# Kernel optimization log

Hardware: AMD Instinct MI355X
Metric: run time of the kernel (lower is better)

The kernel has to match this reference:

```python
import jax, jax.numpy as jnp
import numpy as np

B, V, C, H, W, D = 1, 3, 64, 96, 96, 48


def bilinear_sample(feat, gx, gy):
    """torch F.grid_sample(mode='bilinear', padding_mode='zeros', align_corners=True).
    feat: (B, C, H, W); gx, gy: (B, N) normalized coords in [-1, 1]. Returns (B, C, N)."""
    Bf, Cf, Hf, Wf = feat.shape
    x = (gx + 1.0) * 0.5 * (Wf - 1)
    y = (gy + 1.0) * 0.5 * (Hf - 1)
    x0 = jnp.floor(x)
    y0 = jnp.floor(y)
    wx1 = x - x0
    wy1 = y - y0
    wx0 = 1.0 - wx1
    wy0 = 1.0 - wy1
    flat = feat.reshape(Bf, Cf, Hf * Wf)

    def gather(xi, yi):
        valid = (xi >= 0) & (xi <= Wf - 1) & (yi >= 0) & (yi <= Hf - 1)
        xi_c = jnp.clip(xi, 0, Wf - 1).astype(jnp.int32)
        yi_c = jnp.clip(yi, 0, Hf - 1).astype(jnp.int32)
        idx = (yi_c * Wf + xi_c)[:, None, :]  # (B,1,N), broadcast over C
        return jnp.take_along_axis(flat, idx, axis=2) * valid[:, None, :]

    out = (gather(x0, y0) * (wx0 * wy0)[:, None]
           + gather(x0 + 1, y0) * (wx1 * wy0)[:, None]
           + gather(x0, y0 + 1) * (wx0 * wy1)[:, None]
           + gather(x0 + 1, y0 + 1) * (wx1 * wy1)[:, None])
    return out


def src_grid(proj_mat, depth_values, Hs, Ws):
    """homo_warp grid computation. proj_mat: (B,3,4); depth_values: (B,D).
    Returns normalized gx, gy each of shape (B, D*Hs*Ws)."""
    xs = jnp.arange(Ws, dtype=jnp.float32)
    ys = jnp.arange(Hs, dtype=jnp.float32)
    gx_, gy_ = jnp.meshgrid(xs, ys)  # (Hs, Ws) each
    ref = jnp.stack([gx_.ravel(), gy_.ravel(), jnp.ones(Hs * Ws, jnp.float32)], 0)  # (3, HW)
    R = proj_mat[:, :, :3]
    T = proj_mat[:, :, 3]
    # (B,3,D,HW): R @ p + T / depth
    pts = jnp.einsum('bij,jn->bin', R, ref)[:, :, None, :] + T[:, :, None, None] / depth_values[:, None, :, None]
    xy = pts[:, :2] / pts[:, 2:3]
    gx = xy[:, 0] / ((Ws - 1) / 2.0) - 1.0
    gy = xy[:, 1] / ((Hs - 1) / 2.0) - 1.0
    Bb = proj_mat.shape[0]
    return gx.reshape(Bb, -1), gy.reshape(Bb, -1)


def setup_inputs() -> dict:
    key = jax.random.key(0)
    k1, k2, k3, k4 = jax.random.split(key, 4)
    imgs = jax.random.normal(k1, (B, V, 3, H, W), jnp.float32)
    feats = jax.random.normal(k2, (B, V, C, H, W), jnp.float32)
    # near-identity projections so warped coords land mostly in-range (z ~ 1)
    eye = jnp.broadcast_to(jnp.eye(3, dtype=jnp.float32), (B, V, 3, 3))
    Rn = eye + 0.05 * jax.random.normal(k3, (B, V, 3, 3), jnp.float32)
    Tn = 0.5 * jax.random.normal(jax.random.fold_in(k3, 1), (B, V, 3, 1), jnp.float32)
    proj_mats = jnp.concatenate([Rn, Tn], axis=-1)
    depth_values = 2.0 + 4.0 * jax.random.uniform(k4, (B, D), jnp.float32)
    return {"imgs": imgs, "feats": feats, "proj_mats": proj_mats, "depth_values": depth_values}


def reference(imgs, feats, proj_mats, depth_values):
    Bb, Vv, _, Hh, Ww = imgs.shape
    Cc = feats.shape[2]
    Dd = depth_values.shape[1]
    # ref view volume (broadcast over D)
    ref_volume = jnp.broadcast_to(feats[:, 0][:, :, None], (Bb, Cc, Dd, Hh, Ww))
    volume_sum = ref_volume
    volume_sq_sum = ref_volume ** 2
    mask_sum = jnp.ones((Bb, Dd, Hh, Ww), jnp.float32)  # ref view always in-range
    img_chans = [jnp.broadcast_to(imgs[:, 0][:, :, None], (Bb, 3, Dd, Hh, Ww))]
    for i in range(Vv - 1):  # small fixed number of source views
        gx, gy = src_grid(proj_mats[:, i + 1], depth_values, Hh, Ww)
        wv = bilinear_sample(feats[:, i + 1], gx, gy).reshape(Bb, Cc, Dd, Hh, Ww)
        wi = bilinear_sample(imgs[:, i + 1], gx, gy).reshape(Bb, 3, Dd, Hh, Ww)
        m = ((gx > -1.0) & (gx < 1.0) & (gy > -1.0) & (gy < 1.0)).astype(jnp.float32).reshape(Bb, Dd, Hh, Ww)
        volume_sum = volume_sum + wv
        volume_sq_sum = volume_sq_sum + wv ** 2
        mask_sum = mask_sum + m
        img_chans.append(wi)
    count = 1.0 / mask_sum[:, None]  # (B,1,D,H,W)
    var = volume_sq_sum * count - (volume_sum * count) ** 2  # (B,C,D,H,W)
    img_chans.append(var)
    return jnp.concatenate(img_chans, axis=1)  # (B, 3*V + C, D, H, W)
```

## Files before the change

### kernel.cpp

```cpp
#include <hip/hip_runtime.h>

#define BDIM 256

constexpr int Vv = 3, Cc = 64, Hh = 96, Ww = 96, Dd = 48;
constexpr int HW = Hh * Ww;
constexpr int NPIX = Dd * HW;
constexpr int DHW = Dd * HW;

__device__ __forceinline__ void compute_warp_v(const float* __restrict__ P, float depth,
                                               float xf, float yf,
                                               int offs[4], float wts[4], float& inbf)
{
#pragma clang fp contract(off)
    const float r00 = P[0], r01 = P[1], r02 = P[2],  t0 = P[3];
    const float r10 = P[4], r11 = P[5], r12 = P[6],  t1 = P[7];
    const float r20 = P[8], r21 = P[9], r22 = P[10], t2 = P[11];

    const float px = ((r00 * xf + r01 * yf) + r02) + t0 / depth;
    const float py = ((r10 * xf + r11 * yf) + r12) + t1 / depth;
    const float pz = ((r20 * xf + r21 * yf) + r22) + t2 / depth;

    const float xy0 = px / pz;
    const float xy1 = py / pz;
    const float gx = xy0 / ((float)(Ww - 1) * 0.5f) - 1.0f;
    const float gy = xy1 / ((float)(Hh - 1) * 0.5f) - 1.0f;

    const bool inb = (gx > -1.0f) && (gx < 1.0f) && (gy > -1.0f) && (gy < 1.0f);
    inbf = inb ? 1.0f : 0.0f;

    const float sx = (gx + 1.0f) * 0.5f * (float)(Ww - 1);
    const float sy = (gy + 1.0f) * 0.5f * (float)(Hh - 1);
    const float x0 = floorf(sx), y0 = floorf(sy);
    const float wx1 = sx - x0, wy1 = sy - y0;
    const float wx0 = 1.0f - wx1, wy0 = 1.0f - wy1;

#pragma unroll
    for (int k = 0; k < 4; ++k) {
        const float xi = (k & 1) ? (x0 + 1.0f) : x0;
        const float yi = (k & 2) ? (y0 + 1.0f) : y0;
        const float wk = ((k & 1) ? wx1 : wx0) * ((k & 2) ? wy1 : wy0);
        const bool valid = (xi >= 0.0f) && (xi <= (float)(Ww - 1)) &&
                           (yi >= 0.0f) && (yi <= (float)(Hh - 1));
        const float xc = fminf(fmaxf(xi, 0.0f), (float)(Ww - 1));
        const float yc = fminf(fmaxf(yi, 0.0f), (float)(Hh - 1));
        offs[k] = (int)yc * Ww + (int)xc;
        wts[k] = valid ? wk : 0.0f;
    }
}

__device__ __forceinline__ void compute_warp(const float* __restrict__ proj, float depth,
                                             float xf, float yf,
                                             int offs[2][4], float wts[2][4], float& msum)
{
    msum = 1.0f;
#pragma unroll
    for (int v = 0; v < 2; ++v) {
        float inb;
        compute_warp_v(proj + (v + 1) * 12, depth, xf, yf, offs[v], wts[v], inb);
        msum += inb;
    }
}

__device__ __forceinline__ float var_one(float fr, float a1, float a2, float cnt)
{
    const float s  = fr + a1 + a2;
    const float q  = fr * fr + a1 * a1 + a2 * a2;
    const float sc = s * cnt;
    return q * cnt - sc * sc;
}

__global__ void __launch_bounds__(BDIM) transpose_feats_kernel(const float* __restrict__ feats,
                                                               float* __restrict__ ft)
{
    __shared__ float tile[64][65];
    const int v  = blockIdx.y;
    const int p0 = blockIdx.x * 64;
    const float* src = feats + (size_t)v * Cc * HW;

    const int px = threadIdx.x & 63;
    const int c0 = threadIdx.x >> 6;
#pragma unroll
    for (int c = c0; c < Cc; c += 4)
        tile[c][px] = src[(size_t)c * HW + p0 + px];
    __syncthreads();

    const int cc  = threadIdx.x & 63;
    const int pr0 = threadIdx.x >> 6;
    float* dst = ft + ((size_t)v * HW + p0) * Cc;
#pragma unroll
    for (int p = pr0; p < 64; p += 4)
        dst[p * Cc + cc] = tile[cc][p];
}

__global__ void __launch_bounds__(BDIM) ge_row_kernel(
    const float* __restrict__ imgs, const float* __restrict__ ftr,
    const float* __restrict__ proj, const float* __restrict__ depthv,
    float* __restrict__ out)
{
    __shared__ float s_tile[2][Cc / 2][Ww + 1];
    __shared__ alignas(16) int   s_base[2][2][Ww][4];
    __shared__ alignas(16) float s_wt[2][2][Ww][4];
    __shared__ float s_inb[2][2][Ww];

    const int blk = blockIdx.x;
    const int h   = blk / (Dd / 2);
    const int dq  = blk - h * (Dd / 2);
    const int d0  = dq * 2;
    const int tid = threadIdx.x;
    const int rowb0 = d0 * HW + h * Ww;

    if (tid < 2 * Ww) {
        const int v = (tid >= Ww) ? 1 : 0;
        const int w = tid - v * Ww;
        const float* ib = imgs + (size_t)(v + 1) * 3 * HW;
#pragma unroll
        for (int dd = 0; dd < 2; ++dd) {
            int offs[4];
            float wts[4];
            float inb;
            compute_warp_v(proj + (v + 1) * 12, depthv[d0 + dd], (float)w, (float)h,
                           offs, wts, inb);
            s_inb[v][dd][w] = inb;
#pragma unroll
            for (int k = 0; k < 4; ++k) {
                s_base[v][dd][w][k] = ((v + 1) * HW + offs[k]) * Cc;
                s_wt[v][dd][w][k]   = wts[k];
            }
#pragma unroll
            for (int c = 0; c < 3; ++c) {
                const float* p = ib + (size_t)c * HW;
                const float acc = wts[0] * p[offs[0]] + wts[1] * p[offs[1]] +
                                  wts[2] * p[offs[2]] + wts[3] * p[offs[3]];
                out[(3 * (v + 1) + c) * DHW + rowb0 + dd * HW + w] = acc;
            }
        }
    }
    if (tid < Ww) {
        const int hw = h * Ww + tid;
#pragma unroll
        for (int c = 0; c < 3; ++c) {
            const float val = imgs[c * HW + hw];
            out[c * DHW + rowb0 + tid]      = val;
            out[c * DHW + rowb0 + HW + tid] = val;
        }
    }
    __syncthreads();

    const int wave = tid >> 6;
    const int lane = tid & 63;
    const int sub  = lane >> 3;
    const int cq   = lane & 7;
    const int c4   = cq << 2;
    const int p0   = wave * (Ww / 4);

#pragma unroll
    for (int hc = 0; hc < 2; ++hc) {
        const int ch0 = hc * (Cc / 2);

        for (int i = 0; i < 3; ++i) {
            const int p = p0 + i * 8 + sub;
            const int4   b00 = *reinterpret_cast<const int4*>(&s_base[0][0][p][0]);
            const int4   b10 = *reinterpret_cast<const int4*>(&s_base[1][0][p][0]);
            const int4   b01 = *reinterpret_cast<const int4*>(&s_base[0][1][p][0]);
            const int4   b11 = *reinterpret_cast<const int4*>(&s_base[1][1][p][0]);
            const float4 w00 = *reinterpret_cast<const float4*>(&s_wt[0][0][p][0]);
            const float4 w10 = *reinterpret_cast<const float4*>(&s_wt[1][0][p][0]);
            const float4 w01 = *reinterpret_cast<const float4*>(&s_wt[0][1][p][0]);
            const float4 w11 = *reinterpret_cast<const float4*>(&s_wt[1][1][p][0]);
            const float cnt0 = 1.0f / (1.0f + s_inb[0][0][p] + s_inb[1][0][p]);
            const float cnt1 = 1.0f / (1.0f + s_inb[0][1][p] + s_inb[1][1][p]);

            const float4 fr = *reinterpret_cast<const float4*>(
                ftr + (size_t)(h * Ww + p) * Cc + ch0 + c4);

            const float4 a00 = *reinterpret_cast<const float4*>(ftr + b00.x + ch0 + c4);
            const float4 a01 = *reinterpret_cast<const float4*>(ftr + b00.y + ch0 + c4);
            const float4 a02 = *reinterpret_cast<const float4*>(ftr + b00.z + ch0 + c4);
            const float4 a03 = *reinterpret_cast<const float4*>(ftr + b00.w + ch0 + c4);
            const float4 a10 = *reinterpret_cast<const float4*>(ftr + b10.x + ch0 + c4);
            const float4 a11 = *reinterpret_cast<const float4*>(ftr + b10.y + ch0 + c4);
            const float4 a12 = *reinterpret_cast<const float4*>(ftr + b10.z + ch0 + c4);
            const float4 a13 = *reinterpret_cast<const float4*>(ftr + b10.w + ch0 + c4);
            const float4 c00 = *reinterpret_cast<const float4*>(ftr + b01.x + ch0 + c4);
            const float4 c01 = *reinterpret_cast<const float4*>(ftr + b01.y + ch0 + c4);
            const float4 c02 = *reinterpret_cast<const float4*>(ftr + b01.z + ch0 + c4);
            const float4 c03 = *reinterpret_cast<const float4*>(ftr + b01.w + ch0 + c4);
            const float4 c10 = *reinterpret_cast<const float4*>(ftr + b11.x + ch0 + c4);
            const float4 c11 = *reinterpret_cast<const float4*>(ftr + b11.y + ch0 + c4);
            const float4 c12 = *reinterpret_cast<const float4*>(ftr + b11.z + ch0 + c4);
            const float4 c13 = *reinterpret_cast<const float4*>(ftr + b11.w + ch0 + c4);

#define VAR_LANE(dd, W0, W1, V0a, V0b, V0c, V0d, V1a, V1b, V1c, V1d, CNT)                 \
            {                                                                              \
                {                                                                          \
                    const float a1 = W0.x * V0a.x + W0.y * V0b.x + W0.z * V0c.x + W0.w * V0d.x; \
                    const float a2 = W1.x * V1a.x + W1.y * V1b.x + W1.z * V1c.x + W1.w * V1d.x; \
                    s_tile[dd][c4 + 0][p] = var_one(fr.x, a1, a2, CNT);                    \
                }                                                                          \
                {                                                                          \
                    const float a1 = W0.x * V0a.y + W0.y * V0b.y + W0.z * V0c.y + W0.w * V0d.y; \
                    const float a2 = W1.x * V1a.y + W1.y * V1b.y + W1.z * V1c.y + W1.w * V1d.y; \
                    s_tile[dd][c4 + 1][p] = var_one(fr.y, a1, a2, CNT);                    \
                }                                                                          \
                {                                                                          \
                    const float a1 = W0.x * V0a.z + W0.y * V0b.z + W0.z * V0c.z + W0.w * V0d.z; \
                    const float a2 = W1.x * V1a.z + W1.y * V1b.z + W1.z * V1c.z + W1.w * V1d.z; \
                    s_tile[dd][c4 + 2][p] = var_one(fr.z, a1, a2, CNT);                    \
                }                                                                          \
                {                                                                          \
                    const float a1 = W0.x * V0a.w + W0.y * V0b.w + W0.z * V0c.w + W0.w * V0d.w; \
                    const float a2 = W1.x * V1a.w + W1.y * V1b.w + W1.z * V1c.w + W1.w * V1d.w; \
                    s_tile[dd][c4 + 3][p] = var_one(fr.w, a1, a2, CNT);                    \
                }                                                                          \
            }

            VAR_LANE(0, w00, w10, a00, a01, a02, a03, a10, a11, a12, a13, cnt0)
            VAR_LANE(1, w01, w11, c00, c01, c02, c03, c10, c11, c12, c13, cnt1)
#undef VAR_LANE
        }
        __syncthreads();

#pragma unroll
        for (int j = 0; j < (2 * (Cc / 2) * Ww) / BDIM; ++j) {
            const int idx = tid + j * BDIM;
            const int dd  = idx / ((Cc / 2) * Ww);
            const int r   = idx - dd * ((Cc / 2) * Ww);
            const int cc  = r / Ww;
            const int p   = r - cc * Ww;
            out[(9 + ch0 + cc) * DHW + rowb0 + dd * HW + p] = s_tile[dd][cc][p];
        }
        __syncthreads();
    }
}

__global__ void __launch_bounds__(BDIM) ge_direct_kernel(
    const float* __restrict__ imgs, const float* __restrict__ feats,
    const float* __restrict__ proj, const float* __restrict__ depthv,
    float* __restrict__ out)
{
    const int idx = blockIdx.x * BDIM + threadIdx.x;
    if (idx >= NPIX) return;
    const int w = idx % Ww;
    const int t = idx / Ww;
    const int h = t % Hh;
    const int d = t / Hh;
    const int ohw = h * Ww + w;

    int offs[2][4];
    float wts[2][4];
    float msum;
    compute_warp(proj, depthv[d], (float)w, (float)h, offs, wts, msum);

    const int obase = d * HW + ohw;
#pragma unroll
    for (int c = 0; c < 3; ++c)
        out[c * DHW + obase] = imgs[c * HW + ohw];

#pragma unroll
    for (int v = 0; v < 2; ++v) {
        const float* ib = imgs + (size_t)(v + 1) * 3 * HW;
#pragma unroll
        for (int c = 0; c < 3; ++c) {
            const float* p = ib + (size_t)c * HW;
            const float acc = wts[v][0] * p[offs[v][0]] + wts[v][1] * p[offs[v][1]] +
                              wts[v][2] * p[offs[v][2]] + wts[v][3] * p[offs[v][3]];
            out[(3 * (v + 1) + c) * DHW + obase] = acc;
        }
    }

    const float count = 1.0f / msum;
    const float* f0 = feats;
    const float* f1 = feats + (size_t)Cc * HW;
    const float* f2 = feats + (size_t)2 * Cc * HW;
#pragma unroll 8
    for (int c = 0; c < Cc; ++c) {
        const float fr = f0[(size_t)c * HW + ohw];
        const float* p1 = f1 + (size_t)c * HW;
        const float* p2 = f2 + (size_t)c * HW;
        const float a1 = wts[0][0] * p1[offs[0][0]] + wts[0][1] * p1[offs[0][1]] +
                         wts[0][2] * p1[offs[0][2]] + wts[0][3] * p1[offs[0][3]];
        const float a2 = wts[1][0] * p2[offs[1][0]] + wts[1][1] * p2[offs[1][1]] +
                         wts[1][2] * p2[offs[1][2]] + wts[1][3] * p2[offs[1][3]];
        const float s = fr + a1 + a2;
        const float sq = fr * fr + a1 * a1 + a2 * a2;
        const float sc = s * count;
        out[(3 * Vv + c) * DHW + obase] = sq * count - sc * sc;
    }
}

extern "C" void kernel_launch(void* const* d_in, const int* in_sizes, int n_in,
                              void* d_out, int out_size, void* d_ws, size_t ws_size,
                              hipStream_t stream)
{
    const float* imgs   = (const float*)d_in[0];
    const float* feats  = (const float*)d_in[1];
    const float* proj   = (const float*)d_in[2];
    const float* depthv = (const float*)d_in[3];
    float* out = (float*)d_out;

    const size_t need = (size_t)Vv * HW * Cc * sizeof(float);

    if (ws_size >= need) {
        float* ftr = (float*)d_ws;
        dim3 g1(HW / 64, Vv);
        transpose_feats_kernel<<<g1, BDIM, 0, stream>>>(feats, ftr);
        ge_row_kernel<<<Hh * (Dd / 2), BDIM, 0, stream>>>(imgs, ftr, proj, depthv, out);
    } else {
        const int blocks = (NPIX + BDIM - 1) / BDIM;
        ge_direct_kernel<<<blocks, BDIM, 0, stream>>>(imgs, feats, proj, depthv, out);
    }
}
```

Baseline: 174.6 us.

## Halve shared tile and split depth loop to raise row-kernel occupancy

The variance tile in shared memory is halved by processing the two depth slices one after another instead of together. Each inner iteration now issues 9 gathered float4 loads instead of 17. A launch-bounds hint asks for 5 blocks per CU. The warp-setup phase is spread over all 256 threads instead of 192, with each thread handling one (view, depth, column) item. The aim is lower register and LDS pressure for higher occupancy, at the cost of twice as many barriers and less memory-level parallelism per thread.

```diff
diff --git a/kernel.cpp b/kernel.cpp
--- a/kernel.cpp
+++ b/kernel.cpp
@@ -92,12 +92,12 @@
         dst[p * Cc + cc] = tile[cc][p];
 }
 
-__global__ void __launch_bounds__(BDIM) ge_row_kernel(
+__global__ void __launch_bounds__(BDIM, 5) ge_row_kernel(
     const float* __restrict__ imgs, const float* __restrict__ ftr,
     const float* __restrict__ proj, const float* __restrict__ depthv,
     float* __restrict__ out)
 {
-    __shared__ float s_tile[2][Cc / 2][Ww + 1];
+    __shared__ float s_tile[Cc / 2][Ww + 1];
     __shared__ alignas(16) int   s_base[2][2][Ww][4];
     __shared__ alignas(16) float s_wt[2][2][Ww][4];
     __shared__ float s_inb[2][2][Ww];
@@ -109,30 +109,31 @@
     const int tid = threadIdx.x;
     const int rowb0 = d0 * HW + h * Ww;
 
-    if (tid < 2 * Ww) {
-        const int v = (tid >= Ww) ? 1 : 0;
-        const int w = tid - v * Ww;
+    for (int t = tid; t < 2 * 2 * Ww; t += BDIM) {
+        const int v  = t / (2 * Ww);
+        const int r  = t - v * (2 * Ww);
+        const int dd = r / Ww;
+        const int w  = r - dd * Ww;
+
+        int offs[4];
+        float wts[4];
+        float inb;
+        compute_warp_v(proj + (v + 1) * 12, depthv[d0 + dd], (float)w, (float)h,
+                       offs, wts, inb);
+        s_inb[v][dd][w] = inb;
+#pragma unroll
+        for (int k = 0; k < 4; ++k) {
+            s_base[v][dd][w][k] = ((v + 1) * HW + offs[k]) * Cc;
+            s_wt[v][dd][w][k]   = wts[k];
+        }
+
         const float* ib = imgs + (size_t)(v + 1) * 3 * HW;
 #pragma unroll
-        for (int dd = 0; dd < 2; ++dd) {
-            int offs[4];
-            float wts[4];
-            float inb;
-            compute_warp_v(proj + (v + 1) * 12, depthv[d0 + dd], (float)w, (float)h,
-                           offs, wts, inb);
-            s_inb[v][dd][w] = inb;
-#pragma unroll
-            for (int k = 0; k < 4; ++k) {
-                s_base[v][dd][w][k] = ((v + 1) * HW + offs[k]) * Cc;
-                s_wt[v][dd][w][k]   = wts[k];
-            }
-#pragma unroll
-            for (int c = 0; c < 3; ++c) {
-                const float* p = ib + (size_t)c * HW;
-                const float acc = wts[0] * p[offs[0]] + wts[1] * p[offs[1]] +
-                                  wts[2] * p[offs[2]] + wts[3] * p[offs[3]];
-                out[(3 * (v + 1) + c) * DHW + rowb0 + dd * HW + w] = acc;
-            }
+        for (int c = 0; c < 3; ++c) {
+            const float* p = ib + (size_t)c * HW;
+            const float acc = wts[0] * p[offs[0]] + wts[1] * p[offs[1]] +
+                              wts[2] * p[offs[2]] + wts[3] * p[offs[3]];
+            out[(3 * (v + 1) + c) * DHW + rowb0 + dd * HW + w] = acc;
         }
     }
     if (tid < Ww) {
@@ -156,80 +157,61 @@
 #pragma unroll
     for (int hc = 0; hc < 2; ++hc) {
         const int ch0 = hc * (Cc / 2);
-
-        for (int i = 0; i < 3; ++i) {
-            const int p = p0 + i * 8 + sub;
-            const int4   b00 = *reinterpret_cast<const int4*>(&s_base[0][0][p][0]);
-            const int4   b10 = *reinterpret_cast<const int4*>(&s_base[1][0][p][0]);
-            const int4   b01 = *reinterpret_cast<const int4*>(&s_base[0][1][p][0]);
-            const int4   b11 = *reinterpret_cast<const int4*>(&s_base[1][1][p][0]);
-            const float4 w00 = *reinterpret_cast<const float4*>(&s_wt[0][0][p][0]);
-            const float4 w10 = *reinterpret_cast<const float4*>(&s_wt[1][0][p][0]);
-            const float4 w01 = *reinterpret_cast<const float4*>(&s_wt[0][1][p][0]);
-            const float4 w11 = *reinterpret_cast<const float4*>(&s_wt[1][1][p][0]);
-            const float cnt0 = 1.0f / (1.0f + s_inb[0][0][p] + s_inb[1][0][p]);
-            const float cnt1 = 1.0f / (1.0f + s_inb[0][1][p] + s_inb[1][1][p]);
-
-            const float4 fr = *reinterpret_cast<const float4*>(
-                ftr + (size_t)(h * Ww + p) * Cc + ch0 + c4);
-
-            const float4 a00 = *reinterpret_cast<const float4*>(ftr + b00.x + ch0 + c4);
-            const float4 a01 = *reinterpret_cast<const float4*>(ftr + b00.y + ch0 + c4);
-            const float4 a02 = *reinterpret_cast<const float4*>(ftr + b00.z + ch0 + c4);
-            const float4 a03 = *reinterpret_cast<const float4*>(ftr + b00.w + ch0 + c4);
-            const float4 a10 = *reinterpret_cast<const float4*>(ftr + b10.x + ch0 + c4);
-            const float4 a11 = *reinterpret_cast<const float4*>(ftr + b10.y + ch0 + c4);
-            const float4 a12 = *reinterpret_cast<const float4*>(ftr + b10.z + ch0 + c4);
-            const float4 a13 = *reinterpret_cast<const float4*>(ftr + b10.w + ch0 + c4);
-            const float4 c00 = *reinterpret_cast<const float4*>(ftr + b01.x + ch0 + c4);
-            const float4 c01 = *reinterpret_cast<const float4*>(ftr + b01.y + ch0 + c4);
-            const float4 c02 = *reinterpret_cast<const float4*>(ftr + b01.z + ch0 + c4);
-            const float4 c03 = *reinterpret_cast<const float4*>(ftr + b01.w + ch0 + c4);
-            const float4 c10 = *reinterpret_cast<const float4*>(ftr + b11.x + ch0 + c4);
-            const float4 c11 = *reinterpret_cast<const float4*>(ftr + b11.y + ch0 + c4);
-            const float4 c12 = *reinterpret_cast<const float4*>(ftr + b11.z + ch0 + c4);
-            const float4 c13 = *reinterpret_cast<const float4*>(ftr + b11.w + ch0 + c4);
-
-#define VAR_LANE(dd, W0, W1, V0a, V0b, V0c, V0d, V1a, V1b, V1c, V1d, CNT)                 \
-            {                                                                              \
-                {                                                                          \
-                    const float a1 = W0.x * V0a.x + W0.y * V0b.x + W0.z * V0c.x + W0.w * V0d.x; \
-                    const float a2 = W1.x * V1a.x + W1.y * V1b.x + W1.z * V1c.x + W1.w * V1d.x; \
-                    s_tile[dd][c4 + 0][p] = var_one(fr.x, a1, a2, CNT);                    \
-                }                                                                          \
-                {                                                                          \
-                    const float a1 = W0.x * V0a.y + W0.y * V0b.y + W0.z * V0c.y + W0.w * V0d.y; \
-                    const float a2 = W1.x * V1a.y + W1.y * V1b.y + W1.z * V1c.y + W1.w * V1d.y; \
-                    s_tile[dd][c4 + 1][p] = var_one(fr.y, a1, a2, CNT);                    \
-                }                                                                          \
-                {                                                                          \
-                    const float a1 = W0.x * V0a.z + W0.y * V0b.z + W0.z * V0c.z + W0.w * V0d.z; \
-                    const float a2 = W1.x * V1a.z + W1.y * V1b.z + W1.z * V1c.z + W1.w * V1d.z; \
-                    s_tile[dd][c4 + 2][p] = var_one(fr.z, a1, a2, CNT);                    \
-                }                                                                          \
-                {                                                                          \
-                    const float a1 = W0.x * V0a.w + W0.y * V0b.w + W0.z * V0c.w + W0.w * V0d.w; \
-                    const float a2 = W1.x * V1a.w + W1.y * V1b.w + W1.z * V1c.w + W1.w * V1d.w; \
-                    s_tile[dd][c4 + 3][p] = var_one(fr.w, a1, a2, CNT);                    \
-                }                                                                          \
+        const float* fb = ftr + ch0 + c4;
+
+#pragma unroll
+        for (int dd = 0; dd < 2; ++dd) {
+#pragma unroll
+            for (int i = 0; i < 3; ++i) {
+                const int p = p0 + i * 8 + sub;
+                const float cnt = 1.0f / (1.0f + s_inb[0][dd][p] + s_inb[1][dd][p]);
+                const int4   b0 = *reinterpret_cast<const int4*>(&s_base[0][dd][p][0]);
+                const int4   b1 = *reinterpret_cast<const int4*>(&s_base[1][dd][p][0]);
+                const float4 w0 = *reinterpret_cast<const float4*>(&s_wt[0][dd][p][0]);
+                const float4 w1 = *reinterpret_cast<const float4*>(&s_wt[1][dd][p][0]);
+
+                const float4 fr  = *reinterpret_cast<const float4*>(fb + (size_t)(h * Ww + p) * Cc);
+                const float4 v00 = *reinterpret_cast<const float4*>(fb + b0.x);
+                const float4 v01 = *reinterpret_cast<const float4*>(fb + b0.y);
+                const float4 v02 = *reinterpret_cast<const float4*>(fb + b0.z);
+                const float4 v03 = *reinterpret_cast<const float4*>(fb + b0.w);
+                const float4 v10 = *reinterpret_cast<const float4*>(fb + b1.x);
+                const float4 v11 = *reinterpret_cast<const float4*>(fb + b1.y);
+                const float4 v12 = *reinterpret_cast<const float4*>(fb + b1.z);
+                const float4 v13 = *reinterpret_cast<const float4*>(fb + b1.w);
+
+                {
+                    const float a1 = w0.x * v00.x + w0.y * v01.x + w0.z * v02.x + w0.w * v03.x;
+                    const float a2 = w1.x * v10.x + w1.y * v11.x + w1.z * v12.x + w1.w * v13.x;
+                    s_tile[c4 + 0][p] = var_one(fr.x, a1, a2, cnt);
+                }
+                {
+                    const float a1 = w0.x * v00.y + w0.y * v01.y + w0.z * v02.y + w0.w * v03.y;
+                    const float a2 = w1.x * v10.y + w1.y * v11.y + w1.z * v12.y + w1.w * v13.y;
+                    s_tile[c4 + 1][p] = var_one(fr.y, a1, a2, cnt);
+                }
+                {
+                    const float a1 = w0.x * v00.z + w0.y * v01.z + w0.z * v02.z + w0.w * v03.z;
+                    const float a2 = w1.x * v10.z + w1.y * v11.z + w1.z * v12.z + w1.w * v13.z;
+                    s_tile[c4 + 2][p] = var_one(fr.z, a1, a2, cnt);
+                }
+                {
+                    const float a1 = w0.x * v00.w + w0.y * v01.w + w0.z * v02.w + w0.w * v03.w;
+                    const float a2 = w1.x * v10.w + w1.y * v11.w + w1.z * v12.w + w1.w * v13.w;
+                    s_tile[c4 + 3][p] = var_one(fr.w, a1, a2, cnt);
+                }
             }
-
-            VAR_LANE(0, w00, w10, a00, a01, a02, a03, a10, a11, a12, a13, cnt0)
-            VAR_LANE(1, w01, w11, c00, c01, c02, c03, c10, c11, c12, c13, cnt1)
-#undef VAR_LANE
-        }
-        __syncthreads();
-
-#pragma unroll
-        for (int j = 0; j < (2 * (Cc / 2) * Ww) / BDIM; ++j) {
-            const int idx = tid + j * BDIM;
-            const int dd  = idx / ((Cc / 2) * Ww);
-            const int r   = idx - dd * ((Cc / 2) * Ww);
-            const int cc  = r / Ww;
-            const int p   = r - cc * Ww;
-            out[(9 + ch0 + cc) * DHW + rowb0 + dd * HW + p] = s_tile[dd][cc][p];
-        }
-        __syncthreads();
+            __syncthreads();
+
+#pragma unroll
+            for (int j = 0; j < ((Cc / 2) * Ww) / BDIM; ++j) {
+                const int idx = tid + j * BDIM;
+                const int cc  = idx / Ww;
+                const int p   = idx - cc * Ww;
+                out[(9 + ch0 + cc) * DHW + rowb0 + dd * HW + p] = s_tile[cc][p];
+            }
+            __syncthreads();
+        }
     }
 }
 
```

Result: slower. 200.9 us (+15.1%).
